# Performance work log

Measured on AMD Instinct MI355X. Metric: run time of the kernel, lower is better.

The kernel has to match this reference:

```python
import jax, jax.numpy as jnp
import numpy as np

B, T, H = 16, 512, 768
S = 32            # gold spans per example
L = 50            # max_span_len -> candidate ends per span
NT = 3            # num_types
HS = 4 * H        # span repr size


def setup_inputs() -> dict:
    key = jax.random.key(0)
    ks = jax.random.split(key, 8)
    h = jax.random.normal(ks[0], (B, T, H), dtype=jnp.float32)
    attention_mask = jnp.ones((B, T), dtype=jnp.int32)
    starts = jax.random.randint(ks[1], (B, S), 1, 400).astype(jnp.int32)
    lens = jax.random.randint(ks[2], (B, S), 0, L).astype(jnp.int32)
    ends = starts + lens                      # <= 448 < last_tok=510
    types = jax.random.randint(ks[3], (B, S), 0, NT).astype(jnp.int32)
    W1 = jax.random.normal(ks[4], (HS, HS), dtype=jnp.float32) * (1.0 / np.sqrt(HS))
    b1 = jnp.zeros((HS,), dtype=jnp.float32)
    w_score = jax.random.normal(ks[5], (HS,), dtype=jnp.float32) * (1.0 / np.sqrt(HS))
    b_score = jnp.zeros((1,), dtype=jnp.float32)
    W_type = jax.random.normal(ks[6], (HS, NT), dtype=jnp.float32) * (1.0 / np.sqrt(HS))
    b_type = jnp.zeros((NT,), dtype=jnp.float32)
    return {"h": h, "attention_mask": attention_mask, "span_starts": starts,
            "span_ends": ends, "span_types": types, "W1": W1, "b1": b1,
            "w_score": w_score, "b_score": b_score, "W_type": W_type, "b_type": b_type}


def _span_loss(h, attention_mask, span_starts, span_ends, span_types,
               W1, b1, w_score, b_score, W_type, b_type, type_loss_weight=1.0):
    cls = h[:, 0]                                              # [B,H]
    # prefix sums for O(1) segment means: pre[b,t] = sum h[b,0:t]
    pre = jnp.concatenate([jnp.zeros((B, 1, H), h.dtype), jnp.cumsum(h, axis=1)], axis=1)

    valid_len = attention_mask.sum(axis=1)                     # [B]
    last_tok = jnp.maximum(1, valid_len - 2)                   # [B]

    s = span_starts                                            # [B,S]
    e_gold = span_ends
    gold_idx = e_gold - s                                      # [B,S]
    lt = last_tok[:, None]
    span_valid = (s >= 1) & (s <= lt) & (e_gold >= s) & (e_gold <= lt) & (gold_idx < L)

    e_max = jnp.minimum(s + L - 1, lt)                         # [B,S]
    p = s[..., None] + jnp.arange(L, dtype=s.dtype)            # [B,S,L] candidate ends
    cand_valid = p <= e_max[..., None]

    sc = jnp.clip(s, 0, T - 1)
    pc = jnp.clip(p, 0, T - 1)
    bi2 = jnp.arange(B)[:, None]
    bi3 = jnp.arange(B)[:, None, None]

    h_start = h[bi2, sc]                                       # [B,S,H]
    h_end = h[bi3, pc]                                         # [B,S,L,H]
    seg_len = jnp.maximum(p - s[..., None] + 1, 1).astype(h.dtype)
    h_mean = (pre[bi3, pc + 1] - pre[bi2, sc][:, :, None]) / seg_len[..., None]

    repr_ = jnp.concatenate([
        jnp.broadcast_to(h_start[:, :, None], (B, S, L, H)),
        h_end,
        h_mean,
        jnp.broadcast_to(cls[:, None, None], (B, S, L, H)),
    ], axis=-1)                                                # [B,S,L,4H]

    h1 = jax.nn.gelu(jnp.einsum('bslh,hd->bsld', repr_, W1) + b1, approximate=False)
    scores = jnp.einsum('bsld,d->bsl', h1, w_score) + b_score[0]      # [B,S,L]
    type_logits = jnp.einsum('bsld,dk->bslk', h1, W_type) + b_type    # [B,S,L,NT]

    # end-index CE over valid candidate ends
    masked = jnp.where(cand_valid, scores, jnp.float32(-1e9))
    logp_end = jax.nn.log_softmax(masked, axis=-1)             # [B,S,L]
    gi = jnp.clip(gold_idx, 0, L - 1)
    end_loss = -jnp.take_along_axis(logp_end, gi[..., None], axis=-1)[..., 0]  # [B,S]

    # type CE at the gold end index
    tl_gold = jnp.take_along_axis(type_logits, gi[..., None, None], axis=2)[:, :, 0]  # [B,S,NT]
    logp_t = jax.nn.log_softmax(tl_gold, axis=-1)
    tg = jnp.clip(span_types, 0, NT - 1)
    type_loss = -jnp.take_along_axis(logp_t, tg[..., None], axis=-1)[..., 0]  # [B,S]

    vmask = span_valid.astype(h.dtype)
    n_seg = vmask.sum()
    denom = jnp.maximum(n_seg, 1.0)
    loss_end = jnp.where(n_seg > 0, (end_loss * vmask).sum() / denom, 0.0)
    loss_type = jnp.where(n_seg > 0, (type_loss * vmask).sum() / denom, 0.0)
    return loss_end + type_loss_weight * loss_type


def reference(h, attention_mask, span_starts, span_ends, span_types,
              W1, b1, w_score, b_score, W_type, b_type):
    return _span_loss(h, attention_mask, span_starts, span_ends, span_types,
                      W1, b1, w_score, b_score, W_type, b_type)
```

## Files before the change

kernel.cpp:

```cpp
#include <hip/hip_runtime.h>
#include <hip/hip_bf16.h>
#include <math.h>

#define B_ 16
#define T_ 512
#define H_ 768
#define S_ 32
#define L_ 50
#define NT_ 3
#define HS_ 3072
#define CH_ 32
#define CT_ 16

#define TX_ 456
#define YB2 7296
#define GB 14592
#define CLSB 15104
#define XYROWS 14592
#define AROWS 15232

typedef __attribute__((ext_vector_type(8))) short short8;
typedef __attribute__((ext_vector_type(16))) float float16v;

__device__ __forceinline__ unsigned short f2bf(float f) {
    __hip_bfloat16 b = __float2bfloat16(f);
    return *(unsigned short*)&b;
}
__device__ __forceinline__ float bf2f(unsigned short u) {
    union { unsigned int i; float f; } v; v.i = ((unsigned int)u) << 16; return v.f;
}
__device__ __forceinline__ void load_lds16(const void* g, void* l) {
    __builtin_amdgcn_global_load_lds((__attribute__((address_space(1))) void*)g,
                                     (__attribute__((address_space(3))) void*)l, 16, 0, 0);
}
__device__ __forceinline__ ushort4 pack4(float4 v) {
    ushort4 o; o.x = f2bf(v.x); o.y = f2bf(v.y); o.z = f2bf(v.z); o.w = f2bf(v.w);
    return o;
}

__device__ __forceinline__ float gelu_exact(float v) {
    float a = fabsf(v) * 0.70710678118654752f;
    float t = __builtin_amdgcn_rcpf(fmaf(a, 0.47047f, 1.0f));
    float poly = t * fmaf(t, fmaf(t, 0.7478556f, -0.0958798f), 0.3480242f);
    float e = __builtin_amdgcn_exp2f(a * a * -1.4426950408889634f);
    float erfa = fmaf(-poly, e, 1.0f);
    float erfv = copysignf(erfa, v);
    return 0.5f * v * (1.0f + erfv);
}

__global__ __launch_bounds__(256) void cumsum_pass1(const float4* __restrict__ h4,
                                                    float4* __restrict__ partial) {
    int idx = blockIdx.x * 256 + threadIdx.x;
    int hd4 = idx % 192; int t = idx / 192; int ch = t % CH_; int b = t / CH_;
    const float4* hp = h4 + ((size_t)b * T_ + ch * CT_) * 192 + hd4;
    float4 acc = {0.f, 0.f, 0.f, 0.f};
#pragma unroll
    for (int tt = 0; tt < CT_; tt++) {
        float4 v = hp[(size_t)tt * 192];
        acc.x += v.x; acc.y += v.y; acc.z += v.z; acc.w += v.w;
    }
    partial[idx] = acc;
}

__global__ __launch_bounds__(256) void cumsum_pass3(const float4* __restrict__ h4,
                                                    const float4* __restrict__ partial,
                                                    ushort4* __restrict__ Ab4) {
    int idx = blockIdx.x * 256 + threadIdx.x;
    int hd4 = idx % 192; int t = idx / 192; int ch = t % CH_; int b = t / CH_;
    if (ch * CT_ >= TX_) return;
    float4 acc = {0.f, 0.f, 0.f, 0.f};
#pragma unroll
    for (int c = 0; c < CH_; c++) {
        if (c < ch) {
            float4 v = partial[((size_t)b * CH_ + c) * 192 + hd4];
            acc.x += v.x; acc.y += v.y; acc.z += v.z; acc.w += v.w;
        }
    }
    const float4* hp = h4 + ((size_t)b * T_ + ch * CT_) * 192 + hd4;
    if (ch == 0) {
        ushort4 z = {0, 0, 0, 0};
        Ab4[((size_t)(YB2 + b * TX_)) * 192 + hd4] = z;
    }
#pragma unroll
    for (int tt = 0; tt < CT_; tt++) {
        int t2 = ch * CT_ + tt;
        float4 hv = hp[(size_t)tt * 192];
        if (t2 < TX_)
            Ab4[((size_t)(b * TX_ + t2)) * 192 + hd4] = pack4(hv);
        acc.x += hv.x; acc.y += hv.y; acc.z += hv.z; acc.w += hv.w;
        if (t2 + 1 < TX_)
            Ab4[((size_t)(YB2 + b * TX_ + t2 + 1)) * 192 + hd4] = pack4(acc);
    }
}

__global__ void gather_kernel(const float* __restrict__ h,
                              const int* __restrict__ starts,
                              __hip_bfloat16* __restrict__ Ab) {
    int r = blockIdx.x;
    int src_row, dst_row;
    if (r < B_ * S_) {
        int b = r / S_;
        int sv = starts[r];
        int sc = min(max(sv, 0), T_ - 1);
        src_row = b * T_ + sc;
        dst_row = GB + r;
    } else {
        int b = r - B_ * S_;
        src_row = b * T_;
        dst_row = CLSB + b;
    }
    __hip_bfloat16* dst = Ab + (size_t)dst_row * H_;
    const float* src = h + (size_t)src_row * H_;
    for (int j = threadIdx.x; j < H_; j += 256)
        dst[j] = __float2bfloat16(src[j]);
}

__global__ __launch_bounds__(256) void transpose_w(const float* __restrict__ W1,
                                                   __hip_bfloat16* __restrict__ Wt) {
    __shared__ float tile[64][65];
    int n0 = blockIdx.x * 64, k0 = blockIdx.y * 64;
    int c = threadIdx.x & 63, r0 = threadIdx.x >> 6;
#pragma unroll
    for (int i = 0; i < 16; i++) {
        int r = r0 + i * 4;
        tile[r][c] = W1[(size_t)(k0 + r) * HS_ + n0 + c];
    }
    __syncthreads();
    int p = k0 / H_, kl = k0 % H_;
    __hip_bfloat16* out = Wt + (size_t)p * HS_ * H_;
#pragma unroll
    for (int i = 0; i < 16; i++) {
        int r = r0 + i * 4;
        out[(size_t)(n0 + r) * H_ + kl + c] = __float2bfloat16(tile[c][r]);
    }
}

__global__ __launch_bounds__(256) void mfma_gemm(const __hip_bfloat16* __restrict__ Ab,
                                                 const __hip_bfloat16* __restrict__ Wt,
                                                 __hip_bfloat16* __restrict__ XY,
                                                 float* __restrict__ ST,
                                                 float* __restrict__ CC) {
    constexpr int K = H_;
    __shared__ __hip_bfloat16 As[2 * 128 * 32];
    __shared__ __hip_bfloat16 Bs[2 * 128 * 32];
    int tid = threadIdx.x;
    int wave = tid >> 6, lane = tid & 63;
    int n0 = blockIdx.x * 128, m0 = blockIdx.y * 128;
    int wm = (wave & 1) * 64, wn = (wave >> 1) * 64;

    const __hip_bfloat16* Bt;
    if (m0 < YB2)        Bt = Wt + (size_t)1 * HS_ * H_;
    else if (m0 < GB)    Bt = Wt + (size_t)2 * HS_ * H_;
    else if (m0 < CLSB)  Bt = Wt;
    else                 Bt = Wt + (size_t)3 * HS_ * H_;

    float16v acc[2][2] = {};

    int l31 = lane & 31, lh = lane >> 5;

    for (int k0 = 0; k0 < K; k0 += 64) {
        __syncthreads();
#pragma unroll
        for (int i = 0; i < 4; i++) {
            int cid = i * 256 + wave * 64 + lane;
            int hh = cid >> 9, row = (cid >> 2) & 127, pc = cid & 3;
            int lc = pc ^ ((row >> 1) & 3);
            size_t go = (size_t)row * K + k0 + hh * 32 + lc * 8;
            load_lds16(Ab + (size_t)m0 * K + go,
                       (char*)As + (size_t)(i * 256 + wave * 64) * 16);
            load_lds16(Bt + (size_t)n0 * K + go,
                       (char*)Bs + (size_t)(i * 256 + wave * 64) * 16);
        }
        __syncthreads();

        const short* Asp = (const short*)As;
        const short* Bsp = (const short*)Bs;
#pragma unroll
        for (int kk = 0; kk < 4; kk++) {
            int hh = kk >> 1;
            int lc = 2 * (kk & 1) + lh;
            short8 af[2], bf[2];
#pragma unroll
            for (int mi = 0; mi < 2; mi++) {
                int row = wm + mi * 32 + l31;
                int pc = lc ^ ((row >> 1) & 3);
                af[mi] = *(const short8*)&Asp[(hh * 512 + row * 4 + pc) * 8];
            }
#pragma unroll
            for (int ni = 0; ni < 2; ni++) {
                int row = wn + ni * 32 + l31;
                int pc = lc ^ ((row >> 1) & 3);
                bf[ni] = *(const short8*)&Bsp[(hh * 512 + row * 4 + pc) * 8];
            }
#pragma unroll
            for (int mi = 0; mi < 2; mi++)
#pragma unroll
                for (int ni = 0; ni < 2; ni++)
                    acc[mi][ni] = __builtin_amdgcn_mfma_f32_32x32x16_bf16(
                        af[mi], bf[ni], acc[mi][ni], 0, 0, 0);
        }
    }

#pragma unroll
    for (int mi = 0; mi < 2; mi++) {
#pragma unroll
        for (int ni = 0; ni < 2; ni++) {
            int n = n0 + wn + ni * 32 + l31;
#pragma unroll
            for (int r = 0; r < 16; r++) {
                int m = m0 + wm + mi * 32 + (r & 3) + 8 * (r >> 2) + 4 * lh;
                float v = acc[mi][ni][r];
                if (m < XYROWS) {
                    XY[(size_t)m * HS_ + n] = __float2bfloat16(v);
                } else if (m < CLSB) {
                    ST[(size_t)(m - GB) * HS_ + n] = v;
                } else if (m < CLSB + 16) {
                    CC[(size_t)(m - CLSB) * HS_ + n] = v;
                }
            }
        }
    }
}

__global__ __launch_bounds__(256) void c0_kernel(const float4* __restrict__ ST,
                                                 const float4* __restrict__ CC,
                                                 const float4* __restrict__ b1,
                                                 const float4* __restrict__ w_score,
                                                 ushort4* __restrict__ c0b,
                                                 ushort4* __restrict__ wb16) {
    if (blockIdx.x >= 512 * HS_ / 4 / 256) {
        int i = (blockIdx.x - 512 * HS_ / 4 / 256) * 256 + threadIdx.x;
        wb16[i] = pack4(w_score[i]);
        return;
    }
    int i = blockIdx.x * 256 + threadIdx.x;
    int row = i / (HS_ / 4);
    int b = row >> 5;
    int c4 = i % (HS_ / 4);
    float4 s = ST[i], c = CC[b * (HS_ / 4) + c4], bb = b1[c4];
    float4 v = {s.x + c.x + bb.x, s.y + c.y + bb.y, s.z + c.z + bb.z, s.w + c.w + bb.w};
    c0b[i] = pack4(v);
}

__global__ __launch_bounds__(256) void combine_kernel(
    const unsigned short* __restrict__ c0, const unsigned short* __restrict__ wb16,
    const __hip_bfloat16* __restrict__ XY,
    const float* __restrict__ b_score, const float* __restrict__ W_type,
    const int* __restrict__ starts, const int* __restrict__ ends,
    float* __restrict__ scores, float* __restrict__ tgold) {
    int x = blockIdx.x;
    int b = x & 15, s = x >> 4;
    int bs = b * S_ + s;
    int wave = threadIdx.x >> 6, lane = threadIdx.x & 63;
    int pr = blockIdx.y * 4 + wave;
    if (pr >= L_ / 2) return;
    int l0 = pr * 2, l1 = l0 + 1;
    int sv = starts[bs], ev = ends[bs];
    int gi = min(max(ev - sv, 0), L_ - 1);
    int sc = min(max(sv, 0), TX_ - 1);
    int pc0 = min(max(sv + l0, 0), TX_ - 2);
    int pc1 = min(max(sv + l1, 0), TX_ - 2);
    float inv0 = 1.0f / (float)(l0 + 1);
    float inv1 = 1.0f / (float)(l1 + 1);
    bool isg0 = (l0 == gi), isg1 = (l1 == gi);
    bool anyg = isg0 || isg1;

    const unsigned short* X0 = (const unsigned short*)(XY + (size_t)(b * TX_ + pc0) * HS_);
    const unsigned short* X1 = (const unsigned short*)(XY + (size_t)(b * TX_ + pc1) * HS_);
    const unsigned short* Y0 = (const unsigned short*)(XY + (size_t)(YB2 + b * TX_ + pc0 + 1) * HS_);
    const unsigned short* Y1 = (const unsigned short*)(XY + (size_t)(YB2 + b * TX_ + pc1 + 1) * HS_);
    const unsigned short* Ysr = (const unsigned short*)(XY + (size_t)(YB2 + b * TX_ + sc) * HS_);
    const unsigned short* c0r = c0 + (size_t)bs * HS_;

    float local0 = 0.f, local1 = 0.f, t0 = 0.f, t1 = 0.f, t2 = 0.f;
#pragma unroll
    for (int j = 0; j < 6; j++) {
        int d = j * 512 + lane * 8;
        short8 xv0 = *(const short8*)(X0 + d);
        short8 xv1 = *(const short8*)(X1 + d);
        short8 yv0 = *(const short8*)(Y0 + d);
        short8 yv1 = *(const short8*)(Y1 + d);
        short8 sv8 = *(const short8*)(Ysr + d);
        short8 cv8 = *(const short8*)(c0r + d);
        short8 wv8 = *(const short8*)(wb16 + d);
#pragma unroll
        for (int q = 0; q < 8; q++) {
            float ys = bf2f(((const unsigned short*)&sv8)[q]);
            float cv = bf2f(((const unsigned short*)&cv8)[q]);
            float w  = bf2f(((const unsigned short*)&wv8)[q]);
            float v0 = fmaf(bf2f(((const unsigned short*)&yv0)[q]) - ys, inv0, cv) +
                       bf2f(((const unsigned short*)&xv0)[q]);
            float v1 = fmaf(bf2f(((const unsigned short*)&yv1)[q]) - ys, inv1, cv) +
                       bf2f(((const unsigned short*)&xv1)[q]);
            float g0 = gelu_exact(v0);
            float g1 = gelu_exact(v1);
            local0 = fmaf(g0, w, local0);
            local1 = fmaf(g1, w, local1);
            if (anyg) {
                float gg = isg0 ? g0 : g1;
                t0 = fmaf(gg, W_type[(d + q) * NT_ + 0], t0);
                t1 = fmaf(gg, W_type[(d + q) * NT_ + 1], t1);
                t2 = fmaf(gg, W_type[(d + q) * NT_ + 2], t2);
            }
        }
    }
#pragma unroll
    for (int off = 32; off >= 1; off >>= 1) {
        local0 += __shfl_down(local0, off);
        local1 += __shfl_down(local1, off);
    }
    if (lane == 0) {
        float bs0 = b_score[0];
        scores[(size_t)bs * L_ + l0] = local0 + bs0;
        scores[(size_t)bs * L_ + l1] = local1 + bs0;
    }
    if (anyg) {
#pragma unroll
        for (int off = 32; off >= 1; off >>= 1) {
            t0 += __shfl_down(t0, off);
            t1 += __shfl_down(t1, off);
            t2 += __shfl_down(t2, off);
        }
        if (lane == 0) {
            tgold[bs * NT_ + 0] = t0;
            tgold[bs * NT_ + 1] = t1;
            tgold[bs * NT_ + 2] = t2;
        }
    }
}

__global__ __launch_bounds__(512) void loss_kernel(
    const float* __restrict__ scores, const float* __restrict__ tgold,
    const int* __restrict__ mask, const int* __restrict__ starts,
    const int* __restrict__ ends, const int* __restrict__ types,
    const float* __restrict__ b_type, float* __restrict__ out) {
    __shared__ int svl[B_];
    __shared__ float r[3][8];
    int tid = threadIdx.x;
    int b = tid / S_;
    if (tid < B_) svl[tid] = 0;
    __syncthreads();
    {
        int part = 0;
        const int* mp = mask + tid * 16;
#pragma unroll
        for (int i = 0; i < 16; i++) part += mp[i];
        atomicAdd(&svl[tid / (T_ / 16)], part);
    }
    __syncthreads();
    int vl = svl[b];
    int lt = max(1, vl - 2);
    int sv = starts[tid], ev = ends[tid];
    int gold = ev - sv;
    bool valid = (sv >= 1) && (sv <= lt) && (ev >= sv) && (ev <= lt) && (gold < L_);
    int emax = min(sv + L_ - 1, lt);
    const float* sp = scores + (size_t)tid * L_;
    float m = -1e30f;
    for (int l = 0; l < L_; l++) {
        float v = (sv + l <= emax) ? sp[l] : -1e9f;
        m = fmaxf(m, v);
    }
    float sum = 0.f;
    for (int l = 0; l < L_; l++) {
        float v = (sv + l <= emax) ? sp[l] : -1e9f;
        sum += expf(v - m);
    }
    int gi = min(max(gold, 0), L_ - 1);
    float vg = (sv + gi <= emax) ? sp[gi] : -1e9f;
    float end_loss = (m + logf(sum)) - vg;

    float t0 = tgold[tid * 3 + 0] + b_type[0];
    float t1 = tgold[tid * 3 + 1] + b_type[1];
    float t2 = tgold[tid * 3 + 2] + b_type[2];
    float tm = fmaxf(t0, fmaxf(t1, t2));
    float tsum = expf(t0 - tm) + expf(t1 - tm) + expf(t2 - tm);
    int tg = min(max(types[tid], 0), NT_ - 1);
    float tv = (tg == 0) ? t0 : ((tg == 1) ? t1 : t2);
    float type_loss = (tm + logf(tsum)) - tv;

    float ve = valid ? end_loss : 0.f;
    float vt = valid ? type_loss : 0.f;
    float vc = valid ? 1.f : 0.f;
    for (int off = 32; off >= 1; off >>= 1) {
        ve += __shfl_down(ve, off);
        vt += __shfl_down(vt, off);
        vc += __shfl_down(vc, off);
    }
    if ((tid & 63) == 0) {
        int w = tid >> 6;
        r[0][w] = ve; r[1][w] = vt; r[2][w] = vc;
    }
    __syncthreads();
    if (tid == 0) {
        float se = 0, st = 0, n = 0;
        for (int w = 0; w < 8; w++) { se += r[0][w]; st += r[1][w]; n += r[2][w]; }
        float denom = fmaxf(n, 1.f);
        out[0] = (n > 0.f) ? (se / denom + st / denom) : 0.f;
    }
}

extern "C" void kernel_launch(void* const* d_in, const int* in_sizes, int n_in,
                              void* d_out, int out_size, void* d_ws, size_t ws_size,
                              hipStream_t stream) {
    const float* h       = (const float*)d_in[0];
    const int*   mask    = (const int*)d_in[1];
    const int*   starts  = (const int*)d_in[2];
    const int*   ends    = (const int*)d_in[3];
    const int*   types   = (const int*)d_in[4];
    const float* W1      = (const float*)d_in[5];
    const float* b1      = (const float*)d_in[6];
    const float* w_score = (const float*)d_in[7];
    const float* b_score = (const float*)d_in[8];
    const float* W_type  = (const float*)d_in[9];
    const float* b_type  = (const float*)d_in[10];
    float* out = (float*)d_out;

    char* ws = (char*)d_ws;
    size_t off = 0;
    __hip_bfloat16* Ab = (__hip_bfloat16*)(ws + off); off += (size_t)AROWS * H_ * 2;
    __hip_bfloat16* XY = (__hip_bfloat16*)(ws + off); off += (size_t)XYROWS * HS_ * 2;
    __hip_bfloat16* Wt = (__hip_bfloat16*)(ws + off); off += (size_t)4 * HS_ * H_ * 2;
    float* ST     = (float*)(ws + off);               off += (size_t)512 * HS_ * 4;
    float* CC     = (float*)(ws + off);               off += (size_t)16 * HS_ * 4;
    unsigned short* c0b = (unsigned short*)(ws + off); off += (size_t)512 * HS_ * 2;
    unsigned short* wb16 = (unsigned short*)(ws + off); off += (size_t)HS_ * 2;
    float* scores = (float*)(ws + off);               off += (size_t)B_ * S_ * L_ * 4;
    float* tgold  = (float*)(ws + off);               off += (size_t)B_ * S_ * NT_ * 4;
    float4* partial = (float4*)XY;

    hipLaunchKernelGGL(cumsum_pass1, dim3(B_ * CH_ * 192 / 256), dim3(256), 0, stream,
                       (const float4*)h, partial);
    hipLaunchKernelGGL(cumsum_pass3, dim3(B_ * CH_ * 192 / 256), dim3(256), 0, stream,
                       (const float4*)h, (const float4*)partial, (ushort4*)Ab);
    hipLaunchKernelGGL(gather_kernel, dim3(B_ * S_ + B_), dim3(256), 0, stream, h, starts, Ab);
    hipLaunchKernelGGL(transpose_w, dim3(48, 48), dim3(256), 0, stream, W1, Wt);
    hipLaunchKernelGGL(mfma_gemm, dim3(24, AROWS / 128), dim3(256), 0, stream,
                       Ab, Wt, XY, ST, CC);
    hipLaunchKernelGGL(c0_kernel, dim3(512 * HS_ / 4 / 256 + 3), dim3(256), 0, stream,
                       (const float4*)ST, (const float4*)CC, (const float4*)b1,
                       (const float4*)w_score, (ushort4*)c0b, (ushort4*)wb16);
    hipLaunchKernelGGL(combine_kernel, dim3(B_ * S_, 7), dim3(256), 0, stream,
                       c0b, wb16, XY, b_score, W_type, starts, ends, scores, tgold);
    hipLaunchKernelGGL(loss_kernel, dim3(1), dim3(512), 0, stream,
                       scores, tgold, mask, starts, ends, types, b_type, out);
}
```

Before: 328.0 us.

## Rewrite span GEMM with 256x256 tiles, 4-stage LDS pipeline and XCD-aware mapping

The bf16 MFMA GEMM moves from 128x128 tiles with 256 threads and two barriers per k-step to 256x256 tiles with 512 threads. It uses a 4-slot LDS ring with three k-tiles in flight, paced by explicit vmcnt waits and one barrier per step, and switches to 16x16x32 MFMAs raised by setprio. Workgroups are remapped so consecutive tiles share an XCD for better L2 reuse. Row-segment constants are padded to multiples of 256, which adds some wasted padded rows, and the larger register and LDS footprint (128 KB LDS) may limit occupancy.

```diff
diff --git a/kernel.cpp b/kernel.cpp
--- a/kernel.cpp
+++ b/kernel.cpp
@@ -12,15 +12,17 @@
 #define CH_ 32
 #define CT_ 16
 
-#define TX_ 456
-#define YB2 7296
-#define GB 14592
-#define CLSB 15104
-#define XYROWS 14592
-#define AROWS 15232
+#define TX_ 464
+#define YB2 7424
+#define GB 14848
+#define CLSB 15360
+#define XYROWS 14848
+#define AROWS 15616
+#define NKT 24
+#define SLOT_SH 16384
 
 typedef __attribute__((ext_vector_type(8))) short short8;
-typedef __attribute__((ext_vector_type(16))) float float16v;
+typedef __attribute__((ext_vector_type(4))) float f32x4;
 
 __device__ __forceinline__ unsigned short f2bf(float f) {
     __hip_bfloat16 b = __float2bfloat16(f);
@@ -135,18 +137,69 @@
     }
 }
 
-__global__ __launch_bounds__(256) void mfma_gemm(const __hip_bfloat16* __restrict__ Ab,
-                                                 const __hip_bfloat16* __restrict__ Wt,
-                                                 __hip_bfloat16* __restrict__ XY,
-                                                 float* __restrict__ ST,
-                                                 float* __restrict__ CC) {
-    constexpr int K = H_;
-    __shared__ __hip_bfloat16 As[2 * 128 * 32];
-    __shared__ __hip_bfloat16 Bs[2 * 128 * 32];
+__device__ __forceinline__ void stage_tile(const __hip_bfloat16* __restrict__ Ab,
+                                           const __hip_bfloat16* __restrict__ Bt,
+                                           short* slot, int m0, int n0, int k0, int tid) {
+    int wave = tid >> 6;
+    int row = tid >> 2;
+    int c8 = (tid & 3) * 8;
+    const __hip_bfloat16* ap = Ab + (size_t)(m0 + row) * H_ + k0 + c8;
+    const __hip_bfloat16* bp = Bt + (size_t)(n0 + row) * H_ + k0 + c8;
+    char* la = (char*)slot + wave * 1024;
+    char* lb = (char*)(slot + 8192) + wave * 1024;
+    load_lds16(ap, la);
+    load_lds16(ap + (size_t)128 * H_, la + 8192);
+    load_lds16(bp, lb);
+    load_lds16(bp + (size_t)128 * H_, lb + 8192);
+}
+
+__device__ __forceinline__ void compute_tile(const short* __restrict__ As,
+                                             f32x4 (&acc)[8][4],
+                                             int rA, int rB, int kgo) {
+    const short* Bs = As + 8192;
+    short8 a0[4], a1[4], bfr[4];
+#pragma unroll
+    for (int f = 0; f < 4; ++f)
+        a0[f] = *(const short8*)&As[(rA + f * 16) * 32 + kgo];
+#pragma unroll
+    for (int f = 0; f < 4; ++f)
+        bfr[f] = *(const short8*)&Bs[(rB + f * 16) * 32 + kgo];
+#pragma unroll
+    for (int f = 0; f < 4; ++f)
+        a1[f] = *(const short8*)&As[(rA + 64 + f * 16) * 32 + kgo];
+    __builtin_amdgcn_s_setprio(1);
+#pragma unroll
+    for (int mf = 0; mf < 4; ++mf)
+#pragma unroll
+        for (int nf = 0; nf < 4; ++nf)
+            acc[mf][nf] = __builtin_amdgcn_mfma_f32_16x16x32_bf16(
+                a0[mf], bfr[nf], acc[mf][nf], 0, 0, 0);
+    __builtin_amdgcn_s_setprio(0);
+    __builtin_amdgcn_s_setprio(1);
+#pragma unroll
+    for (int mf = 0; mf < 4; ++mf)
+#pragma unroll
+        for (int nf = 0; nf < 4; ++nf)
+            acc[4 + mf][nf] = __builtin_amdgcn_mfma_f32_16x16x32_bf16(
+                a1[mf], bfr[nf], acc[4 + mf][nf], 0, 0, 0);
+    __builtin_amdgcn_s_setprio(0);
+}
+
+__global__ __launch_bounds__(512, 2) void mfma_gemm(const __hip_bfloat16* __restrict__ Ab,
+                                                    const __hip_bfloat16* __restrict__ Wt,
+                                                    __hip_bfloat16* __restrict__ XY,
+                                                    float* __restrict__ ST,
+                                                    float* __restrict__ CC) {
+    __shared__ short lds[4 * SLOT_SH];
     int tid = threadIdx.x;
     int wave = tid >> 6, lane = tid & 63;
-    int n0 = blockIdx.x * 128, m0 = blockIdx.y * 128;
-    int wm = (wave & 1) * 64, wn = (wave >> 1) * 64;
+    int wr = wave >> 2, wc = wave & 3;
+
+    int orig = blockIdx.x;
+    int xcd = orig & 7, loc = orig >> 3;
+    int wg = (xcd < 4 ? xcd * 92 : 368 + (xcd - 4) * 91) + loc;
+    int mt = wg / 12, nt = wg - mt * 12;
+    int m0 = mt << 8, n0 = nt << 8;
 
     const __hip_bfloat16* Bt;
     if (m0 < YB2)        Bt = Wt + (size_t)1 * HS_ * H_;
@@ -154,62 +207,50 @@
     else if (m0 < CLSB)  Bt = Wt;
     else                 Bt = Wt + (size_t)3 * HS_ * H_;
 
-    float16v acc[2][2] = {};
-
-    int l31 = lane & 31, lh = lane >> 5;
-
-    for (int k0 = 0; k0 < K; k0 += 64) {
-        __syncthreads();
-#pragma unroll
-        for (int i = 0; i < 4; i++) {
-            int cid = i * 256 + wave * 64 + lane;
-            int hh = cid >> 9, row = (cid >> 2) & 127, pc = cid & 3;
-            int lc = pc ^ ((row >> 1) & 3);
-            size_t go = (size_t)row * K + k0 + hh * 32 + lc * 8;
-            load_lds16(Ab + (size_t)m0 * K + go,
-                       (char*)As + (size_t)(i * 256 + wave * 64) * 16);
-            load_lds16(Bt + (size_t)n0 * K + go,
-                       (char*)Bs + (size_t)(i * 256 + wave * 64) * 16);
-        }
-        __syncthreads();
-
-        const short* Asp = (const short*)As;
-        const short* Bsp = (const short*)Bs;
-#pragma unroll
-        for (int kk = 0; kk < 4; kk++) {
-            int hh = kk >> 1;
-            int lc = 2 * (kk & 1) + lh;
-            short8 af[2], bf[2];
-#pragma unroll
-            for (int mi = 0; mi < 2; mi++) {
-                int row = wm + mi * 32 + l31;
-                int pc = lc ^ ((row >> 1) & 3);
-                af[mi] = *(const short8*)&Asp[(hh * 512 + row * 4 + pc) * 8];
-            }
-#pragma unroll
-            for (int ni = 0; ni < 2; ni++) {
-                int row = wn + ni * 32 + l31;
-                int pc = lc ^ ((row >> 1) & 3);
-                bf[ni] = *(const short8*)&Bsp[(hh * 512 + row * 4 + pc) * 8];
-            }
-#pragma unroll
-            for (int mi = 0; mi < 2; mi++)
-#pragma unroll
-                for (int ni = 0; ni < 2; ni++)
-                    acc[mi][ni] = __builtin_amdgcn_mfma_f32_32x32x16_bf16(
-                        af[mi], bf[ni], acc[mi][ni], 0, 0, 0);
-        }
-    }
-
-#pragma unroll
-    for (int mi = 0; mi < 2; mi++) {
-#pragma unroll
-        for (int ni = 0; ni < 2; ni++) {
-            int n = n0 + wn + ni * 32 + l31;
-#pragma unroll
-            for (int r = 0; r < 16; r++) {
-                int m = m0 + wm + mi * 32 + (r & 3) + 8 * (r >> 2) + 4 * lh;
-                float v = acc[mi][ni][r];
+    f32x4 acc[8][4] = {};
+
+    for (int t = 0; t < 3; ++t)
+        stage_tile(Ab, Bt, lds + t * SLOT_SH, m0, n0, t * 32, tid);
+
+    int l15 = lane & 15;
+    int kgo = (lane >> 4) * 8;
+    int rA = wr * 128 + l15;
+    int rB = wc * 64 + l15;
+
+    for (int kt = 0; kt < NKT - 3; ++kt) {
+        asm volatile("s_waitcnt vmcnt(8)" ::: "memory");
+        __builtin_amdgcn_s_barrier();
+        __builtin_amdgcn_sched_barrier(0);
+        stage_tile(Ab, Bt, lds + ((kt + 3) & 3) * SLOT_SH, m0, n0, (kt + 3) * 32, tid);
+        compute_tile(lds + (kt & 3) * SLOT_SH, acc, rA, rB, kgo);
+        __builtin_amdgcn_sched_barrier(0);
+    }
+    asm volatile("s_waitcnt vmcnt(8)" ::: "memory");
+    __builtin_amdgcn_s_barrier();
+    __builtin_amdgcn_sched_barrier(0);
+    compute_tile(lds + ((NKT - 3) & 3) * SLOT_SH, acc, rA, rB, kgo);
+    __builtin_amdgcn_sched_barrier(0);
+    asm volatile("s_waitcnt vmcnt(4)" ::: "memory");
+    __builtin_amdgcn_s_barrier();
+    __builtin_amdgcn_sched_barrier(0);
+    compute_tile(lds + ((NKT - 2) & 3) * SLOT_SH, acc, rA, rB, kgo);
+    __builtin_amdgcn_sched_barrier(0);
+    asm volatile("s_waitcnt vmcnt(0)" ::: "memory");
+    __builtin_amdgcn_s_barrier();
+    __builtin_amdgcn_sched_barrier(0);
+    compute_tile(lds + ((NKT - 1) & 3) * SLOT_SH, acc, rA, rB, kgo);
+
+    int mb = m0 + wr * 128, nb = n0 + wc * 64;
+#pragma unroll
+    for (int mf = 0; mf < 8; ++mf) {
+#pragma unroll
+        for (int nf = 0; nf < 4; ++nf) {
+            int n = nb + nf * 16 + l15;
+            int mr = mb + mf * 16 + (lane >> 4) * 4;
+#pragma unroll
+            for (int r = 0; r < 4; ++r) {
+                int m = mr + r;
+                float v = acc[mf][nf][r];
                 if (m < XYROWS) {
                     XY[(size_t)m * HS_ + n] = __float2bfloat16(v);
                 } else if (m < CLSB) {
@@ -434,7 +475,7 @@
                        (const float4*)h, (const float4*)partial, (ushort4*)Ab);
     hipLaunchKernelGGL(gather_kernel, dim3(B_ * S_ + B_), dim3(256), 0, stream, h, starts, Ab);
     hipLaunchKernelGGL(transpose_w, dim3(48, 48), dim3(256), 0, stream, W1, Wt);
-    hipLaunchKernelGGL(mfma_gemm, dim3(24, AROWS / 128), dim3(256), 0, stream,
+    hipLaunchKernelGGL(mfma_gemm, dim3((AROWS / 256) * 12), dim3(512), 0, stream,
                        Ab, Wt, XY, ST, CC);
     hipLaunchKernelGGL(c0_kernel, dim3(512 * HS_ / 4 / 256 + 3), dim3(256), 0, stream,
                        (const float4*)ST, (const float4*)CC, (const float4*)b1,
```

Result: faster. 319.0 us (-2.7%).
